# Kernel optimization log

Measured on AMD Instinct MI355X. Metric: run time of the kernel, lower is better.

## Reference

```python
import jax, jax.numpy as jnp
import numpy as np

N_HEADS = 8
TANH_CLIP = 10.0


def setup_inputs() -> dict:
    key = jax.random.key(0)
    ks = jax.random.split(key, 7)
    B, N, D = 128, 1000, 512
    embeddings = jax.random.normal(ks[0], (B, N, D), dtype=jnp.float32)
    step_context = jax.random.normal(ks[1], (B, 1, 2 * D), dtype=jnp.float32)
    # action mask: True = feasible action; guarantee at least one feasible per row
    action_mask = jax.random.uniform(ks[2], (B, 1, N)) > 0.3
    action_mask = action_mask.at[:, :, 0].set(True)
    s = 0.02
    W_node = jax.random.normal(ks[3], (D, 3 * D), dtype=jnp.float32) * s
    W_fixed = jax.random.normal(ks[4], (D, D), dtype=jnp.float32) * s
    W_step = jax.random.normal(ks[5], (2 * D, D), dtype=jnp.float32) * s
    W_out = jax.random.normal(ks[6], (D, D), dtype=jnp.float32) * s
    return {"embeddings": embeddings, "step_context": step_context,
            "action_mask": action_mask, "W_node": W_node, "W_fixed": W_fixed,
            "W_step": W_step, "W_out": W_out}


def reference(embeddings, step_context, action_mask, W_node, W_fixed, W_step, W_out):
    B, N, D = embeddings.shape
    H = N_HEADS
    hd = D // H
    neg_inf = jnp.float32(-jnp.inf)

    # --- precompute (Decoder._precompute) ---
    graph_embed = embeddings.mean(axis=1)                      # [B, D]
    kvl = embeddings @ W_node                                  # [B, N, 3D]
    _gk, gv, logit_key = jnp.split(kvl, 3, axis=-1)
    # source bug: glimpse_key variable is overwritten with glimpse_val, and
    # attention is called with key = value = glimpse_val
    KV = gv.reshape(B, N, H, hd).transpose(0, 2, 1, 3)         # [B, H, N, hd]
    graph_context = (graph_embed @ W_fixed)[:, None, :]        # [B, 1, D]

    # --- per-step query (Decoder._get_log_p) ---
    query = graph_context + step_context @ W_step              # [B, 1, D]
    q = query.reshape(B, 1, H, hd).transpose(0, 2, 1, 3)       # [B, H, 1, hd]

    # --- inner MHA (scaled_dot_product_attention with boolean mask) ---
    scores = jnp.einsum('bhqs,bhns->bhqn', q, KV) / jnp.sqrt(jnp.float32(hd))
    scores = jnp.where(action_mask[:, None, :, :], scores, neg_inf)  # [B,H,1,N]
    attn = jax.nn.softmax(scores, axis=-1)
    heads = jnp.einsum('bhqn,bhns->bhqs', attn, KV)            # [B, H, 1, hd]
    heads = heads.transpose(0, 2, 1, 3).reshape(B, 1, D)       # [B, 1, D]

    # --- glimpse projection and logit head ---
    glimpse = heads @ W_out                                    # [B, 1, D]
    logits = jnp.einsum('bqd,bnd->bqn', glimpse, logit_key) / jnp.sqrt(jnp.float32(D))
    logits = jnp.tanh(logits) * TANH_CLIP
    logits = jnp.where(action_mask, logits, neg_inf)
    return jax.nn.log_softmax(logits, axis=-1)                 # [B, 1, N]
```

## Files before the change

### kernel.cpp

```cpp
#include <hip/hip_runtime.h>
#include <math.h>

#define B 128
#define N 1000
#define D 512
#define H 8
#define NCHUNK 8
#define CHUNK 125

#define OFF_PMEAN   0
#define OFF_QW      (OFF_PMEAN + B*NCHUNK*D)
#define OFF_PAE     (OFF_QW + B*D*H)
#define OFF_ZC      (OFF_PAE + B*NCHUNK*H*D)
#define OFF_GW      (OFF_ZC + B*NCHUNK*H)
#define OFF_LG      (OFF_GW + B*D)
#define OFF_LMAX    (OFF_LG + B*N)
#define OFF_LSUM    (OFF_LMAX + B*NCHUNK)

__global__ void k1_partial_mean(const float* __restrict__ emb, float* __restrict__ ws){
    int chunk = blockIdx.x, b = blockIdx.y, t = threadIdx.x;
    const float4* e4 = (const float4*)emb;
    float4 acc = make_float4(0.f, 0.f, 0.f, 0.f);
    size_t rowbase = ((size_t)b * N + (size_t)chunk * CHUNK) * (D / 4);
    for (int n = 0; n < CHUNK; ++n) {
        float4 v = e4[rowbase + (size_t)n * (D / 4) + t];
        acc.x += v.x; acc.y += v.y; acc.z += v.z; acc.w += v.w;
    }
    float4* o = (float4*)(ws + OFF_PMEAN + (size_t)(b * NCHUNK + chunk) * D);
    o[t] = acc;
}

__global__ void k2_prep(const float* __restrict__ stepc, const float* __restrict__ Wnode,
                        const float* __restrict__ Wfix, const float* __restrict__ Wstep,
                        float* __restrict__ ws){
    int b = blockIdx.x, d = threadIdx.x;
    __shared__ float ge[D];
    __shared__ float q[D];
    float s = 0.f;
    #pragma unroll
    for (int c = 0; c < NCHUNK; ++c) s += ws[OFF_PMEAN + (size_t)(b * NCHUNK + c) * D + d];
    ge[d] = s * (1.0f / N);
    __syncthreads();
    float a0 = 0.f, a1 = 0.f, a2 = 0.f, a3 = 0.f;
    for (int k = 0; k < D; k += 4) {
        a0 = fmaf(ge[k],     Wfix[(size_t)k * D + d],       a0);
        a1 = fmaf(ge[k + 1], Wfix[(size_t)(k + 1) * D + d], a1);
        a2 = fmaf(ge[k + 2], Wfix[(size_t)(k + 2) * D + d], a2);
        a3 = fmaf(ge[k + 3], Wfix[(size_t)(k + 3) * D + d], a3);
    }
    const float* sc = stepc + (size_t)b * 2 * D;
    for (int k = 0; k < 2 * D; k += 4) {
        a0 = fmaf(sc[k],     Wstep[(size_t)k * D + d],       a0);
        a1 = fmaf(sc[k + 1], Wstep[(size_t)(k + 1) * D + d], a1);
        a2 = fmaf(sc[k + 2], Wstep[(size_t)(k + 2) * D + d], a2);
        a3 = fmaf(sc[k + 3], Wstep[(size_t)(k + 3) * D + d], a3);
    }
    q[d] = (a0 + a1) + (a2 + a3);
    __syncthreads();
    const float* wrow = Wnode + (size_t)d * 3 * D + D;
    float* outp = ws + OFF_QW + ((size_t)b * D + d) * H;
    #pragma unroll
    for (int h = 0; h < H; ++h) {
        float a = 0.f;
        const float* qh = q + h * 64;
        const float* wh = wrow + h * 64;
        #pragma unroll 8
        for (int s2 = 0; s2 < 64; ++s2) a = fmaf(qh[s2], wh[s2], a);
        outp[h] = a;
    }
}

__global__ __launch_bounds__(128) void kc2_attn(const float* __restrict__ emb,
        const unsigned char* __restrict__ mask, float* __restrict__ ws){
    const int cg = blockIdx.x, b = blockIdx.y, t = threadIdx.x;
    __shared__ float qws[D * H];
    __shared__ float p[H][128];
    {
        const float4* qg = (const float4*)(ws + OFF_QW + (size_t)b * D * H);
        float4* qs4 = (float4*)qws;
        #pragma unroll
        for (int i = 0; i < 8; ++i) qs4[i * 128 + t] = qg[i * 128 + t];
    }
    __syncthreads();
    {
        float a[H];
        #pragma unroll
        for (int h = 0; h < H; ++h) a[h] = 0.f;
        if (t < CHUNK) {
            const int n = cg * CHUNK + t;
            const float4* e4 = (const float4*)(emb + ((size_t)b * N + n) * D);
            for (int d4 = 0; d4 < D / 4; ++d4) {
                float4 e = e4[d4];
                #pragma unroll
                for (int j = 0; j < 4; ++j) {
                    float ev = (j == 0) ? e.x : (j == 1) ? e.y : (j == 2) ? e.z : e.w;
                    const float4* qp = (const float4*)&qws[(d4 * 4 + j) * H];
                    float4 q0 = qp[0], q1 = qp[1];
                    a[0] = fmaf(ev, q0.x, a[0]); a[1] = fmaf(ev, q0.y, a[1]);
                    a[2] = fmaf(ev, q0.z, a[2]); a[3] = fmaf(ev, q0.w, a[3]);
                    a[4] = fmaf(ev, q1.x, a[4]); a[5] = fmaf(ev, q1.y, a[5]);
                    a[6] = fmaf(ev, q1.z, a[6]); a[7] = fmaf(ev, q1.w, a[7]);
                }
            }
            bool m = mask[(size_t)b * N + n] != 0;
            #pragma unroll
            for (int h = 0; h < H; ++h)
                p[h][t] = m ? __expf(a[h] * 0.125f) : 0.f;
        } else {
            #pragma unroll
            for (int h = 0; h < H; ++h) p[h][t] = 0.f;
        }
    }
    __syncthreads();
    {
        int h = t >> 4, j = t & 15;
        float z = 0.f;
        for (int i = j; i < 128; i += 16) z += p[h][i];
        #pragma unroll
        for (int o = 8; o > 0; o >>= 1) z += __shfl_xor(z, o);
        if (j == 0) ws[OFF_ZC + ((size_t)b * NCHUNK + cg) * H + h] = z;
    }
    {
        float4 acc[H];
        #pragma unroll
        for (int h = 0; h < H; ++h) acc[h] = make_float4(0.f, 0.f, 0.f, 0.f);
        const float4* ecol = (const float4*)(emb + ((size_t)b * N + (size_t)cg * CHUNK) * D) + t;
        for (int i = 0; i < CHUNK; ++i) {
            float4 e = ecol[(size_t)i * (D / 4)];
            #pragma unroll
            for (int h = 0; h < H; ++h) {
                float w = p[h][i];
                acc[h].x = fmaf(w, e.x, acc[h].x);
                acc[h].y = fmaf(w, e.y, acc[h].y);
                acc[h].z = fmaf(w, e.z, acc[h].z);
                acc[h].w = fmaf(w, e.w, acc[h].w);
            }
        }
        float4* paeb = (float4*)(ws + OFF_PAE + (((size_t)b * NCHUNK + cg) * H) * (size_t)D);
        #pragma unroll
        for (int h = 0; h < H; ++h) paeb[(size_t)h * (D / 4) + t] = acc[h];
    }
}

__global__ __launch_bounds__(512) void kd_post(const float* __restrict__ Wnode,
        const float* __restrict__ Wout, float* __restrict__ ws){
    int b = blockIdx.x, t = threadIdx.x;
    __shared__ float ae[H * D];
    __shared__ float heads[D];
    __shared__ float gl[D];
    __shared__ float iZ[H];
    if (t < H) {
        float Z = 0.f;
        #pragma unroll
        for (int c = 0; c < NCHUNK; ++c)
            Z += ws[OFF_ZC + ((size_t)b * NCHUNK + c) * H + t];
        iZ[t] = 1.0f / Z;
    }
    __syncthreads();
    #pragma unroll
    for (int h = 0; h < H; ++h) {
        float s = 0.f;
        #pragma unroll
        for (int c = 0; c < NCHUNK; ++c)
            s += ws[OFF_PAE + (((size_t)b * NCHUNK + c) * H + h) * (size_t)D + t];
        ae[h * D + t] = s * iZ[h];
    }
    __syncthreads();
    {
        int h = t >> 6;
        const float* aeh = ae + h * D;
        const float* col = Wnode + 512 + t;
        float a0 = 0.f, a1 = 0.f, a2 = 0.f, a3 = 0.f;
        for (int d = 0; d < D; d += 4) {
            a0 = fmaf(aeh[d],     col[(size_t)d * (3 * D)],       a0);
            a1 = fmaf(aeh[d + 1], col[(size_t)(d + 1) * (3 * D)], a1);
            a2 = fmaf(aeh[d + 2], col[(size_t)(d + 2) * (3 * D)], a2);
            a3 = fmaf(aeh[d + 3], col[(size_t)(d + 3) * (3 * D)], a3);
        }
        heads[t] = (a0 + a1) + (a2 + a3);
    }
    __syncthreads();
    {
        float a0 = 0.f, a1 = 0.f, a2 = 0.f, a3 = 0.f;
        for (int d = 0; d < D; d += 4) {
            a0 = fmaf(heads[d],     Wout[(size_t)d * D + t],       a0);
            a1 = fmaf(heads[d + 1], Wout[(size_t)(d + 1) * D + t], a1);
            a2 = fmaf(heads[d + 2], Wout[(size_t)(d + 2) * D + t], a2);
            a3 = fmaf(heads[d + 3], Wout[(size_t)(d + 3) * D + t], a3);
        }
        gl[t] = (a0 + a1) + (a2 + a3);
    }
    __syncthreads();
    {
        const float* wrow = Wnode + (size_t)t * (3 * D) + 2 * D;
        float a0 = 0.f, a1 = 0.f, a2 = 0.f, a3 = 0.f;
        for (int e = 0; e < D; e += 4) {
            a0 = fmaf(gl[e],     wrow[e],     a0);
            a1 = fmaf(gl[e + 1], wrow[e + 1], a1);
            a2 = fmaf(gl[e + 2], wrow[e + 2], a2);
            a3 = fmaf(gl[e + 3], wrow[e + 3], a3);
        }
        ws[OFF_GW + (size_t)b * D + t] = (a0 + a1) + (a2 + a3);
    }
}

__global__ void k7_logits(const float* __restrict__ emb, const unsigned char* __restrict__ mask,
                          float* __restrict__ ws){
    int chunk = blockIdx.x, b = blockIdx.y, t = threadIdx.x;
    __shared__ float4 gw4[D / 4];
    __shared__ float rmax[2], rsum[2];
    gw4[t] = ((const float4*)(ws + OFF_GW + (size_t)b * D))[t];
    __syncthreads();
    float lg = -INFINITY;
    int n = chunk * CHUNK + t;
    if (t < CHUNK) {
        const float4* e4 = (const float4*)(emb + ((size_t)b * N + n) * D);
        float a0 = 0.f, a1 = 0.f, a2 = 0.f, a3 = 0.f;
        for (int d4 = 0; d4 < D / 4; ++d4) {
            float4 e = e4[d4];
            float4 g = gw4[d4];
            a0 = fmaf(e.x, g.x, a0); a1 = fmaf(e.y, g.y, a1);
            a2 = fmaf(e.z, g.z, a2); a3 = fmaf(e.w, g.w, a3);
        }
        float accv = (a0 + a1) + (a2 + a3);
        bool m = mask[(size_t)b * N + n] != 0;
        lg = m ? tanhf(accv * 0.044194173824159216f) * 10.0f : -INFINITY;
        ws[OFF_LG + (size_t)b * N + n] = lg;
    }
    float mx = lg;
    #pragma unroll
    for (int o = 32; o > 0; o >>= 1) mx = fmaxf(mx, __shfl_xor(mx, o));
    if ((t & 63) == 0) rmax[t >> 6] = mx;
    __syncthreads();
    float bm = fmaxf(rmax[0], rmax[1]);
    float term = (lg == -INFINITY) ? 0.f : __expf(lg - bm);
    #pragma unroll
    for (int o = 32; o > 0; o >>= 1) term += __shfl_xor(term, o);
    if ((t & 63) == 0) rsum[t >> 6] = term;
    __syncthreads();
    if (t == 0) {
        ws[OFF_LMAX + (size_t)b * NCHUNK + chunk] = bm;
        ws[OFF_LSUM + (size_t)b * NCHUNK + chunk] = rsum[0] + rsum[1];
    }
}

__global__ void k8_out(const float* __restrict__ ws, float* __restrict__ out){
    int b = blockIdx.x, t = threadIdx.x;
    __shared__ float Ls;
    if (t == 0) {
        float M = -INFINITY;
        #pragma unroll
        for (int c = 0; c < NCHUNK; ++c)
            M = fmaxf(M, ws[OFF_LMAX + (size_t)b * NCHUNK + c]);
        float S = 0.f;
        #pragma unroll
        for (int c = 0; c < NCHUNK; ++c) {
            float m = ws[OFF_LMAX + (size_t)b * NCHUNK + c];
            if (m != -INFINITY) S += __expf(m - M) * ws[OFF_LSUM + (size_t)b * NCHUNK + c];
        }
        Ls = M + __logf(S);
    }
    __syncthreads();
    float L = Ls;
    for (int j = t; j < N; j += 256)
        out[(size_t)b * N + j] = fmaxf(ws[OFF_LG + (size_t)b * N + j] - L, -1e30f);
}

extern "C" void kernel_launch(void* const* d_in, const int* in_sizes, int n_in,
                              void* d_out, int out_size, void* d_ws, size_t ws_size,
                              hipStream_t stream) {
    const float* emb   = (const float*)d_in[0];
    const float* stepc = (const float*)d_in[1];
    const unsigned char* mask = (const unsigned char*)d_in[2];
    const float* Wnode = (const float*)d_in[3];
    const float* Wfix  = (const float*)d_in[4];
    const float* Wstep = (const float*)d_in[5];
    const float* Wout  = (const float*)d_in[6];
    float* out = (float*)d_out;
    float* ws  = (float*)d_ws;

    k1_partial_mean<<<dim3(NCHUNK, B), 128, 0, stream>>>(emb, ws);
    k2_prep<<<dim3(B), 512, 0, stream>>>(stepc, Wnode, Wfix, Wstep, ws);
    kc2_attn<<<dim3(NCHUNK, B), 128, 0, stream>>>(emb, mask, ws);
    kd_post<<<dim3(B), 512, 0, stream>>>(Wnode, Wout, ws);
    k7_logits<<<dim3(NCHUNK, B), 128, 0, stream>>>(emb, mask, ws);
    k8_out<<<dim3(B), 256, 0, stream>>>(ws, out);
}
```

Measured before the change: 350.2 us.

## Use wave-per-row coalesced loads in attention and logit kernels, finer mean chunks

The attention-score and logit kernels change from one thread per embedding row, where each thread strides through its own row with uncoalesced accesses, to one 64-lane wave per row. Each lane handles 8 contiguous floats, and results are combined with a shuffle reduction. The attention kernel keeps q in registers and does the weighted-sum pass with 256 threads over float2 columns. The logits kernel uses an online max/sum. The mean kernel is split into 20 chunks of 50 rows for more parallelism. The aim is to fix poor memory coalescing on the 262MB embedding reads, at the cost of shuffle-reduction overhead and higher register pressure.

Result: slower. 390.4 us (+11.5%).

```diff
diff --git a/kernel.cpp b/kernel.cpp
--- a/kernel.cpp
+++ b/kernel.cpp
@@ -5,29 +5,31 @@
 #define N 1000
 #define D 512
 #define H 8
-#define NCHUNK 8
-#define CHUNK 125
-
-#define OFF_PMEAN   0
-#define OFF_QW      (OFF_PMEAN + B*NCHUNK*D)
-#define OFF_PAE     (OFF_QW + B*D*H)
-#define OFF_ZC      (OFF_PAE + B*NCHUNK*H*D)
-#define OFF_GW      (OFF_ZC + B*NCHUNK*H)
-#define OFF_LG      (OFF_GW + B*D)
-#define OFF_LMAX    (OFF_LG + B*N)
-#define OFF_LSUM    (OFF_LMAX + B*NCHUNK)
+#define NCH 8
+#define CHK 125
+#define NCHM 20
+#define CHKM 50
+#define WPB 4
+
+#define OFF_PMEAN 0
+#define OFF_QW    (OFF_PMEAN + B*NCHM*D)
+#define OFF_PAE   (OFF_QW + B*D*H)
+#define OFF_ZC    (OFF_PAE + B*NCH*H*D)
+#define OFF_GW    (OFF_ZC + B*NCH*H)
+#define OFF_LG    (OFF_GW + B*D)
+#define OFF_LMAX  (OFF_LG + B*N)
+#define OFF_LSUM  (OFF_LMAX + B*NCH)
 
 __global__ void k1_partial_mean(const float* __restrict__ emb, float* __restrict__ ws){
     int chunk = blockIdx.x, b = blockIdx.y, t = threadIdx.x;
-    const float4* e4 = (const float4*)emb;
+    const float4* e4 = (const float4*)emb + ((size_t)b * N + (size_t)chunk * CHKM) * (D / 4) + t;
     float4 acc = make_float4(0.f, 0.f, 0.f, 0.f);
-    size_t rowbase = ((size_t)b * N + (size_t)chunk * CHUNK) * (D / 4);
-    for (int n = 0; n < CHUNK; ++n) {
-        float4 v = e4[rowbase + (size_t)n * (D / 4) + t];
+    #pragma unroll 2
+    for (int n = 0; n < CHKM; ++n) {
+        float4 v = e4[(size_t)n * (D / 4)];
         acc.x += v.x; acc.y += v.y; acc.z += v.z; acc.w += v.w;
     }
-    float4* o = (float4*)(ws + OFF_PMEAN + (size_t)(b * NCHUNK + chunk) * D);
-    o[t] = acc;
+    ((float4*)(ws + OFF_PMEAN + (size_t)(b * NCHM + chunk) * D))[t] = acc;
 }
 
 __global__ void k2_prep(const float* __restrict__ stepc, const float* __restrict__ Wnode,
@@ -38,7 +40,7 @@
     __shared__ float q[D];
     float s = 0.f;
     #pragma unroll
-    for (int c = 0; c < NCHUNK; ++c) s += ws[OFF_PMEAN + (size_t)(b * NCHUNK + c) * D + d];
+    for (int c = 0; c < NCHM; ++c) s += ws[OFF_PMEAN + (size_t)(b * NCHM + c) * D + d];
     ge[d] = s * (1.0f / N);
     __syncthreads();
     float a0 = 0.f, a1 = 0.f, a2 = 0.f, a3 = 0.f;
@@ -70,75 +72,75 @@
     }
 }
 
-__global__ __launch_bounds__(128) void kc2_attn(const float* __restrict__ emb,
+__global__ __launch_bounds__(256) void kb_attn(const float* __restrict__ emb,
         const unsigned char* __restrict__ mask, float* __restrict__ ws){
     const int cg = blockIdx.x, b = blockIdx.y, t = threadIdx.x;
-    __shared__ float qws[D * H];
-    __shared__ float p[H][128];
-    {
-        const float4* qg = (const float4*)(ws + OFF_QW + (size_t)b * D * H);
-        float4* qs4 = (float4*)qws;
-        #pragma unroll
-        for (int i = 0; i < 8; ++i) qs4[i * 128 + t] = qg[i * 128 + t];
-    }
-    __syncthreads();
-    {
-        float a[H];
-        #pragma unroll
-        for (int h = 0; h < H; ++h) a[h] = 0.f;
-        if (t < CHUNK) {
-            const int n = cg * CHUNK + t;
-            const float4* e4 = (const float4*)(emb + ((size_t)b * N + n) * D);
-            for (int d4 = 0; d4 < D / 4; ++d4) {
-                float4 e = e4[d4];
-                #pragma unroll
-                for (int j = 0; j < 4; ++j) {
-                    float ev = (j == 0) ? e.x : (j == 1) ? e.y : (j == 2) ? e.z : e.w;
-                    const float4* qp = (const float4*)&qws[(d4 * 4 + j) * H];
-                    float4 q0 = qp[0], q1 = qp[1];
-                    a[0] = fmaf(ev, q0.x, a[0]); a[1] = fmaf(ev, q0.y, a[1]);
-                    a[2] = fmaf(ev, q0.z, a[2]); a[3] = fmaf(ev, q0.w, a[3]);
-                    a[4] = fmaf(ev, q1.x, a[4]); a[5] = fmaf(ev, q1.y, a[5]);
-                    a[6] = fmaf(ev, q1.z, a[6]); a[7] = fmaf(ev, q1.w, a[7]);
-                }
-            }
-            bool m = mask[(size_t)b * N + n] != 0;
+    const int w = t >> 6, l = t & 63;
+    __shared__ float p_lds[128][H];
+    float4 qv[16];
+    {
+        const float4* q4 = (const float4*)(ws + OFF_QW + (size_t)b * D * H) + l * 16;
+        #pragma unroll
+        for (int j = 0; j < 16; ++j) qv[j] = q4[j];
+    }
+    const float* embb = emb + ((size_t)b * N + (size_t)cg * CHK) * D;
+    const unsigned char* mb = mask + (size_t)b * N + cg * CHK;
+    for (int nl = w; nl < CHK; nl += WPB) {
+        const float4* er = (const float4*)(embb + (size_t)nl * D) + l * 2;
+        float4 e0 = er[0], e1 = er[1];
+        float part[8];
+        #pragma unroll
+        for (int h = 0; h < 8; ++h) part[h] = 0.f;
+#define ACCJ(j, ev) { \
+        part[0] = fmaf(ev, qv[2*(j)].x, part[0]); part[1] = fmaf(ev, qv[2*(j)].y, part[1]); \
+        part[2] = fmaf(ev, qv[2*(j)].z, part[2]); part[3] = fmaf(ev, qv[2*(j)].w, part[3]); \
+        part[4] = fmaf(ev, qv[2*(j)+1].x, part[4]); part[5] = fmaf(ev, qv[2*(j)+1].y, part[5]); \
+        part[6] = fmaf(ev, qv[2*(j)+1].z, part[6]); part[7] = fmaf(ev, qv[2*(j)+1].w, part[7]); }
+        ACCJ(0, e0.x) ACCJ(1, e0.y) ACCJ(2, e0.z) ACCJ(3, e0.w)
+        ACCJ(4, e1.x) ACCJ(5, e1.y) ACCJ(6, e1.z) ACCJ(7, e1.w)
+#undef ACCJ
+        #pragma unroll
+        for (int o = 32; o > 0; o >>= 1) {
             #pragma unroll
-            for (int h = 0; h < H; ++h)
-                p[h][t] = m ? __expf(a[h] * 0.125f) : 0.f;
-        } else {
-            #pragma unroll
-            for (int h = 0; h < H; ++h) p[h][t] = 0.f;
-        }
-    }
-    __syncthreads();
-    {
-        int h = t >> 4, j = t & 15;
+            for (int h = 0; h < 8; ++h) part[h] += __shfl_xor(part[h], o);
+        }
+        bool m = mb[nl] != 0;
+        float pe[8];
+        #pragma unroll
+        for (int h = 0; h < 8; ++h) pe[h] = m ? __expf(part[h] * 0.125f) : 0.f;
+        if (l == 0) {
+            *(float4*)&p_lds[nl][0] = make_float4(pe[0], pe[1], pe[2], pe[3]);
+            *(float4*)&p_lds[nl][4] = make_float4(pe[4], pe[5], pe[6], pe[7]);
+        }
+    }
+    __syncthreads();
+    if (t < H) {
         float z = 0.f;
-        for (int i = j; i < 128; i += 16) z += p[h][i];
-        #pragma unroll
-        for (int o = 8; o > 0; o >>= 1) z += __shfl_xor(z, o);
-        if (j == 0) ws[OFF_ZC + ((size_t)b * NCHUNK + cg) * H + h] = z;
-    }
-    {
-        float4 acc[H];
-        #pragma unroll
-        for (int h = 0; h < H; ++h) acc[h] = make_float4(0.f, 0.f, 0.f, 0.f);
-        const float4* ecol = (const float4*)(emb + ((size_t)b * N + (size_t)cg * CHUNK) * D) + t;
-        for (int i = 0; i < CHUNK; ++i) {
-            float4 e = ecol[(size_t)i * (D / 4)];
-            #pragma unroll
-            for (int h = 0; h < H; ++h) {
-                float w = p[h][i];
-                acc[h].x = fmaf(w, e.x, acc[h].x);
-                acc[h].y = fmaf(w, e.y, acc[h].y);
-                acc[h].z = fmaf(w, e.z, acc[h].z);
-                acc[h].w = fmaf(w, e.w, acc[h].w);
-            }
-        }
-        float4* paeb = (float4*)(ws + OFF_PAE + (((size_t)b * NCHUNK + cg) * H) * (size_t)D);
-        #pragma unroll
-        for (int h = 0; h < H; ++h) paeb[(size_t)h * (D / 4) + t] = acc[h];
+        for (int i = 0; i < CHK; ++i) z += p_lds[i][t];
+        ws[OFF_ZC + ((size_t)b * NCH + cg) * H + t] = z;
+    }
+    {
+        float2 acc[8];
+        #pragma unroll
+        for (int h = 0; h < 8; ++h) acc[h] = make_float2(0.f, 0.f);
+        const float2* ecol = (const float2*)embb + t;
+        #pragma unroll 2
+        for (int i = 0; i < CHK; ++i) {
+            float2 e = ecol[(size_t)i * (D / 2)];
+            float4 pa = *(const float4*)&p_lds[i][0];
+            float4 pb = *(const float4*)&p_lds[i][4];
+            acc[0].x = fmaf(pa.x, e.x, acc[0].x); acc[0].y = fmaf(pa.x, e.y, acc[0].y);
+            acc[1].x = fmaf(pa.y, e.x, acc[1].x); acc[1].y = fmaf(pa.y, e.y, acc[1].y);
+            acc[2].x = fmaf(pa.z, e.x, acc[2].x); acc[2].y = fmaf(pa.z, e.y, acc[2].y);
+            acc[3].x = fmaf(pa.w, e.x, acc[3].x); acc[3].y = fmaf(pa.w, e.y, acc[3].y);
+            acc[4].x = fmaf(pb.x, e.x, acc[4].x); acc[4].y = fmaf(pb.x, e.y, acc[4].y);
+            acc[5].x = fmaf(pb.y, e.x, acc[5].x); acc[5].y = fmaf(pb.y, e.y, acc[5].y);
+            acc[6].x = fmaf(pb.z, e.x, acc[6].x); acc[6].y = fmaf(pb.z, e.y, acc[6].y);
+            acc[7].x = fmaf(pb.w, e.x, acc[7].x); acc[7].y = fmaf(pb.w, e.y, acc[7].y);
+        }
+        float2* paeb = (float2*)(ws + OFF_PAE) + ((size_t)(b * NCH + cg) * H) * (D / 2) + t;
+        #pragma unroll
+        for (int h = 0; h < 8; ++h) paeb[(size_t)h * (D / 2)] = acc[h];
     }
 }
 
@@ -152,8 +154,8 @@
     if (t < H) {
         float Z = 0.f;
         #pragma unroll
-        for (int c = 0; c < NCHUNK; ++c)
-            Z += ws[OFF_ZC + ((size_t)b * NCHUNK + c) * H + t];
+        for (int c = 0; c < NCH; ++c)
+            Z += ws[OFF_ZC + ((size_t)b * NCH + c) * H + t];
         iZ[t] = 1.0f / Z;
     }
     __syncthreads();
@@ -161,8 +163,8 @@
     for (int h = 0; h < H; ++h) {
         float s = 0.f;
         #pragma unroll
-        for (int c = 0; c < NCHUNK; ++c)
-            s += ws[OFF_PAE + (((size_t)b * NCHUNK + c) * H + h) * (size_t)D + t];
+        for (int c = 0; c < NCH; ++c)
+            s += ws[OFF_PAE + (((size_t)b * NCH + c) * H + h) * (size_t)D + t];
         ae[h * D + t] = s * iZ[h];
     }
     __syncthreads();
@@ -204,43 +206,50 @@
     }
 }
 
-__global__ void k7_logits(const float* __restrict__ emb, const unsigned char* __restrict__ mask,
-                          float* __restrict__ ws){
-    int chunk = blockIdx.x, b = blockIdx.y, t = threadIdx.x;
-    __shared__ float4 gw4[D / 4];
-    __shared__ float rmax[2], rsum[2];
-    gw4[t] = ((const float4*)(ws + OFF_GW + (size_t)b * D))[t];
-    __syncthreads();
-    float lg = -INFINITY;
-    int n = chunk * CHUNK + t;
-    if (t < CHUNK) {
-        const float4* e4 = (const float4*)(emb + ((size_t)b * N + n) * D);
-        float a0 = 0.f, a1 = 0.f, a2 = 0.f, a3 = 0.f;
-        for (int d4 = 0; d4 < D / 4; ++d4) {
-            float4 e = e4[d4];
-            float4 g = gw4[d4];
-            a0 = fmaf(e.x, g.x, a0); a1 = fmaf(e.y, g.y, a1);
-            a2 = fmaf(e.z, g.z, a2); a3 = fmaf(e.w, g.w, a3);
-        }
-        float accv = (a0 + a1) + (a2 + a3);
-        bool m = mask[(size_t)b * N + n] != 0;
-        lg = m ? tanhf(accv * 0.044194173824159216f) * 10.0f : -INFINITY;
-        ws[OFF_LG + (size_t)b * N + n] = lg;
-    }
-    float mx = lg;
-    #pragma unroll
-    for (int o = 32; o > 0; o >>= 1) mx = fmaxf(mx, __shfl_xor(mx, o));
-    if ((t & 63) == 0) rmax[t >> 6] = mx;
-    __syncthreads();
-    float bm = fmaxf(rmax[0], rmax[1]);
-    float term = (lg == -INFINITY) ? 0.f : __expf(lg - bm);
-    #pragma unroll
-    for (int o = 32; o > 0; o >>= 1) term += __shfl_xor(term, o);
-    if ((t & 63) == 0) rsum[t >> 6] = term;
+__global__ __launch_bounds__(256) void kc_logits(const float* __restrict__ emb,
+        const unsigned char* __restrict__ mask, float* __restrict__ ws){
+    const int cg = blockIdx.x, b = blockIdx.y, t = threadIdx.x;
+    const int w = t >> 6, l = t & 63;
+    __shared__ float wm[WPB], wsum[WPB];
+    float4 g0, g1;
+    {
+        const float4* g4 = (const float4*)(ws + OFF_GW + (size_t)b * D) + l * 2;
+        g0 = g4[0]; g1 = g4[1];
+    }
+    const float* embb = emb + ((size_t)b * N + (size_t)cg * CHK) * D;
+    const unsigned char* mb = mask + (size_t)b * N + cg * CHK;
+    float m = -INFINITY, s = 0.f;
+    for (int nl = w; nl < CHK; nl += WPB) {
+        const float4* er = (const float4*)(embb + (size_t)nl * D) + l * 2;
+        float4 e0 = er[0], e1 = er[1];
+        float a0 = fmaf(e0.x, g0.x, 0.f), a1 = fmaf(e0.y, g0.y, 0.f);
+        float a2 = fmaf(e0.z, g0.z, 0.f), a3 = fmaf(e0.w, g0.w, 0.f);
+        a0 = fmaf(e1.x, g1.x, a0); a1 = fmaf(e1.y, g1.y, a1);
+        a2 = fmaf(e1.z, g1.z, a2); a3 = fmaf(e1.w, g1.w, a3);
+        float a = (a0 + a1) + (a2 + a3);
+        #pragma unroll
+        for (int o = 32; o > 0; o >>= 1) a += __shfl_xor(a, o);
+        bool mk = mb[nl] != 0;
+        float lg = mk ? tanhf(a * 0.044194173824159216f) * 10.0f : -INFINITY;
+        if (l == 0) ws[OFF_LG + (size_t)b * N + cg * CHK + nl] = lg;
+        if (lg != -INFINITY) {
+            float mn = fmaxf(m, lg);
+            s = s * __expf(m - mn) + __expf(lg - mn);
+            m = mn;
+        }
+    }
+    if (l == 0) { wm[w] = m; wsum[w] = s; }
     __syncthreads();
     if (t == 0) {
-        ws[OFF_LMAX + (size_t)b * NCHUNK + chunk] = bm;
-        ws[OFF_LSUM + (size_t)b * NCHUNK + chunk] = rsum[0] + rsum[1];
+        float M = -INFINITY;
+        #pragma unroll
+        for (int i = 0; i < WPB; ++i) M = fmaxf(M, wm[i]);
+        float S = 0.f;
+        #pragma unroll
+        for (int i = 0; i < WPB; ++i)
+            if (wm[i] != -INFINITY) S += wsum[i] * __expf(wm[i] - M);
+        ws[OFF_LMAX + (size_t)b * NCH + cg] = M;
+        ws[OFF_LSUM + (size_t)b * NCH + cg] = S;
     }
 }
 
@@ -250,13 +259,13 @@
     if (t == 0) {
         float M = -INFINITY;
         #pragma unroll
-        for (int c = 0; c < NCHUNK; ++c)
-            M = fmaxf(M, ws[OFF_LMAX + (size_t)b * NCHUNK + c]);
+        for (int c = 0; c < NCH; ++c)
+            M = fmaxf(M, ws[OFF_LMAX + (size_t)b * NCH + c]);
         float S = 0.f;
         #pragma unroll
-        for (int c = 0; c < NCHUNK; ++c) {
-            float m = ws[OFF_LMAX + (size_t)b * NCHUNK + c];
-            if (m != -INFINITY) S += __expf(m - M) * ws[OFF_LSUM + (size_t)b * NCHUNK + c];
+        for (int c = 0; c < NCH; ++c) {
+            float m = ws[OFF_LMAX + (size_t)b * NCH + c];
+            if (m != -INFINITY) S += __expf(m - M) * ws[OFF_LSUM + (size_t)b * NCH + c];
         }
         Ls = M + __logf(S);
     }
@@ -279,10 +288,10 @@
     float* out = (float*)d_out;
     float* ws  = (float*)d_ws;
 
-    k1_partial_mean<<<dim3(NCHUNK, B), 128, 0, stream>>>(emb, ws);
+    k1_partial_mean<<<dim3(NCHM, B), 128, 0, stream>>>(emb, ws);
     k2_prep<<<dim3(B), 512, 0, stream>>>(stepc, Wnode, Wfix, Wstep, ws);
-    kc2_attn<<<dim3(NCHUNK, B), 128, 0, stream>>>(emb, mask, ws);
+    kb_attn<<<dim3(NCH, B), 256, 0, stream>>>(emb, mask, ws);
     kd_post<<<dim3(B), 512, 0, stream>>>(Wnode, Wout, ws);
-    k7_logits<<<dim3(NCHUNK, B), 128, 0, stream>>>(emb, mask, ws);
+    kc_logits<<<dim3(NCH, B), 256, 0, stream>>>(emb, mask, ws);
     k8_out<<<dim3(B), 256, 0, stream>>>(ws, out);
 }
```
